# Optimization experiments

Measured on AMD Instinct MI355X. Metric: run time of the kernel, lower is better.

Reference implementation:

```python
import jax, jax.numpy as jnp
import numpy as np

B, S, D = 2, 2048, 4096
NH, NKV = 32, 8
HD = D // NH  # 128
N_REP = NH // NKV  # 4


def setup_inputs() -> dict:
    key = jax.random.key(0)
    ks = jax.random.split(key, 5)
    scale = 0.02
    return {
        "x": jax.random.normal(ks[0], (B, S, D), dtype=jnp.float32),
        "wq": jax.random.normal(ks[1], (D, NH * HD), dtype=jnp.float32) * scale,
        "wk": jax.random.normal(ks[2], (D, NKV * HD), dtype=jnp.float32) * scale,
        "wv": jax.random.normal(ks[3], (D, NKV * HD), dtype=jnp.float32) * scale,
        "wo": jax.random.normal(ks[4], (NH * HD, D), dtype=jnp.float32) * scale,
    }


def reference(x, wq, wk, wv, wo):
    bsz, toks, _ = x.shape
    q = (x @ wq).reshape(bsz, toks, NH, HD)      # [B,S,NH,HD]
    k = (x @ wk).reshape(bsz, toks, NKV, HD)     # [B,S,NKV,HD]
    v = (x @ wv).reshape(bsz, toks, NKV, HD)
    # GQA: fold n_rep into einsum instead of materializing repeated K/V.
    qg = q.reshape(bsz, toks, NKV, N_REP, HD)    # group query heads per kv head
    scores = jnp.einsum('bqgrd,bkgd->bgrqk', qg, k) / jnp.sqrt(jnp.asarray(HD, x.dtype))
    attn = jax.nn.softmax(scores.astype(jnp.float32), axis=-1).astype(x.dtype)
    out = jnp.einsum('bgrqk,bkgd->bqgrd', attn, v)  # [B,S,NKV,N_REP,HD]
    out = out.reshape(bsz, toks, NH * HD)
    return out @ wo
```

## Files before the change

### kernel.cpp

```cpp
#include <hip/hip_runtime.h>
#include <math.h>

typedef _Float16 f16;
using f16x8 = __attribute__((ext_vector_type(8))) _Float16;
using f32x4 = __attribute__((ext_vector_type(4))) float;

#define BATCH 2
#define SEQ   2048
#define DMODEL 4096
#define NH    32
#define NKV   8
#define HD    128
#define MTOK  (BATCH*SEQ)

__global__ __launch_bounds__(256) void prep_k(const float* __restrict__ x, f16* __restrict__ xh,
                                              const float* __restrict__ wq, f16* __restrict__ wqT,
                                              const float* __restrict__ wk, const float* __restrict__ wv,
                                              f16* __restrict__ wkvT,
                                              const float* __restrict__ wo, f16* __restrict__ woT,
                                              float scale) {
  __shared__ float tile[32][33];
  const int bid = blockIdx.x, t = threadIdx.x;
  if (bid < 8192) {
    const int i = bid * 256 + t;
    const float4* p = reinterpret_cast<const float4*>(x) + (size_t)i * 2;
    float4 a = p[0], b = p[1];
    f16x8 o = { (f16)a.x, (f16)a.y, (f16)a.z, (f16)a.w,
                (f16)b.x, (f16)b.y, (f16)b.z, (f16)b.w };
    reinterpret_cast<f16x8*>(xh)[i] = o;
    return;
  }
  const float* w; f16* dst; int Nd; float sc;
  int bb;
  if (bid < 24576)      { bb = bid - 8192;  w = wq; dst = wqT;  Nd = DMODEL; sc = scale; }
  else if (bid < 32768) { bb = bid - 24576; const int z = bb >> 12; bb &= 4095;
                          w = z ? wv : wk; dst = wkvT + (size_t)z * 1024 * DMODEL; Nd = 1024; sc = 1.0f; }
  else                  { bb = bid - 32768; w = wo; dst = woT; Nd = DMODEL; sc = 1.0f; }
  const int ntile = Nd >> 5;
  const int n0 = (bb % ntile) * 32, k0 = (bb / ntile) * 32;
  const int r = t >> 3, c4 = (t & 7) << 2;
  const float4 v = *reinterpret_cast<const float4*>(w + (size_t)(k0 + r) * Nd + n0 + c4);
  tile[r][c4 + 0] = v.x; tile[r][c4 + 1] = v.y; tile[r][c4 + 2] = v.z; tile[r][c4 + 3] = v.w;
  __syncthreads();
  union { f16 h[4]; ushort4 u4; } pk;
  pk.h[0] = (f16)(tile[c4 + 0][r] * sc);
  pk.h[1] = (f16)(tile[c4 + 1][r] * sc);
  pk.h[2] = (f16)(tile[c4 + 2][r] * sc);
  pk.h[3] = (f16)(tile[c4 + 3][r] * sc);
  *reinterpret_cast<ushort4*>(dst + (size_t)(n0 + r) * DMODEL + k0 + c4) = pk.u4;
}

__global__ __launch_bounds__(256) void transpose_cvt_k(const float* __restrict__ w,
                                                       f16* __restrict__ wt, int Kd, int Nd,
                                                       float scale) {
  __shared__ float tile[32][33];
  const int t = threadIdx.x;
  const int n0 = blockIdx.x * 32, k0 = blockIdx.y * 32;
  const int r = t >> 3, c4 = (t & 7) << 2;
  const float4 v = *reinterpret_cast<const float4*>(w + (size_t)(k0 + r) * Nd + n0 + c4);
  tile[r][c4 + 0] = v.x; tile[r][c4 + 1] = v.y; tile[r][c4 + 2] = v.z; tile[r][c4 + 3] = v.w;
  __syncthreads();
  union { f16 h[4]; ushort4 u4; } pk;
  pk.h[0] = (f16)(tile[c4 + 0][r] * scale);
  pk.h[1] = (f16)(tile[c4 + 1][r] * scale);
  pk.h[2] = (f16)(tile[c4 + 2][r] * scale);
  pk.h[3] = (f16)(tile[c4 + 3][r] * scale);
  *reinterpret_cast<ushort4*>(wt + (size_t)(n0 + r) * Kd + k0 + c4) = pk.u4;
}

__global__ __launch_bounds__(256) void transpose_cvt2_k(const float* __restrict__ w0,
                                                        const float* __restrict__ w1,
                                                        f16* __restrict__ wt, int Kd, int Nd) {
  __shared__ float tile[32][33];
  const float* w = blockIdx.z ? w1 : w0;
  f16* dst = wt + (size_t)blockIdx.z * Nd * Kd;
  const int t = threadIdx.x;
  const int n0 = blockIdx.x * 32, k0 = blockIdx.y * 32;
  const int r = t >> 3, c4 = (t & 7) << 2;
  const float4 v = *reinterpret_cast<const float4*>(w + (size_t)(k0 + r) * Nd + n0 + c4);
  tile[r][c4 + 0] = v.x; tile[r][c4 + 1] = v.y; tile[r][c4 + 2] = v.z; tile[r][c4 + 3] = v.w;
  __syncthreads();
  union { f16 h[4]; ushort4 u4; } pk;
  pk.h[0] = (f16)tile[c4 + 0][r];
  pk.h[1] = (f16)tile[c4 + 1][r];
  pk.h[2] = (f16)tile[c4 + 2][r];
  pk.h[3] = (f16)tile[c4 + 3][r];
  *reinterpret_cast<ushort4*>(dst + (size_t)(n0 + r) * Kd + k0 + c4) = pk.u4;
}

__global__ __launch_bounds__(256) void cvt_f32_f16_k(const float* __restrict__ in,
                                                     f16* __restrict__ out, int n8) {
  int i = blockIdx.x * 256 + threadIdx.x;
  if (i >= n8) return;
  const float4* p = reinterpret_cast<const float4*>(in) + (size_t)i * 2;
  float4 a = p[0], b = p[1];
  f16x8 o = { (f16)a.x, (f16)a.y, (f16)a.z, (f16)a.w,
              (f16)b.x, (f16)b.y, (f16)b.z, (f16)b.w };
  reinterpret_cast<f16x8*>(out)[i] = o;
}

__global__ __launch_bounds__(512, 2) void gemm_kv8_k(const f16* __restrict__ A,
                                                     const f16* __restrict__ BT,
                                                     f16* __restrict__ Kc,
                                                     f16* __restrict__ Vt,
                                                     int M, int N, int K) {
  __shared__ f16 lds[2 * 24576];
  char* ldsb = (char*)lds;

  const int t = threadIdx.x, lane = t & 63, w = t >> 6;
  const int wm = w >> 2, wn = w & 3;
  const int ll = lane & 15, lg = lane >> 4;
  const int nbn = N >> 8;
  const int nwg = gridDim.x, cpx = nwg >> 3, bid = blockIdx.x;
  const int swz = (bid & 7) * cpx + (bid >> 3);
  const int bm = swz / nbn, bn = swz % nbn;
  const size_t m0 = (size_t)bm << 7, n0 = (size_t)bn << 8;
  const int NT = K >> 6;

  const int uoff[4] = {0, 8192, 16384, 32768};

  auto stage = [&](int bufI, int unit, int ktS) {
    char* dstb = ldsb + (size_t)bufI * 49152 + uoff[unit];
    if (unit < 2) {
      const f16* base = A + (m0 + (size_t)(unit & 1) * 64) * (size_t)K;
      const int row = t >> 3, lin = t & 7;
      const int slot = lin ^ (row & 7);
      const f16* src = base + (size_t)row * K + ktS + slot * 8;
      __builtin_amdgcn_global_load_lds((const __attribute__((address_space(1))) void*)src,
          (__attribute__((address_space(3))) void*)(dstb + (size_t)t * 16), 16, 0, 0);
    } else {
      const f16* base = BT + (n0 + (size_t)(unit & 1) * 128) * (size_t)K;
#pragma unroll
      for (int rr = 0; rr < 2; rr++) {
        const int u = t + rr * 512;
        const int row = u >> 3, lin = u & 7;
        const int slot = lin ^ (row & 7);
        const f16* src = base + (size_t)row * K + ktS + slot * 8;
        __builtin_amdgcn_global_load_lds((const __attribute__((address_space(1))) void*)src,
            (__attribute__((address_space(3))) void*)(dstb + (size_t)u * 16), 16, 0, 0);
      }
    }
  };

  f32x4 acc[4][4];
#pragma unroll
  for (int i = 0; i < 4; i++)
#pragma unroll
    for (int j = 0; j < 4; j++) acc[i][j] = f32x4{0.f, 0.f, 0.f, 0.f};

  f16x8 af[2][2];
  f16x8 bfr[2][2][2];

  stage(0, 0, 0); stage(0, 1, 0); stage(0, 2, 0); stage(0, 3, 0);
  stage(1, 0, 64); stage(1, 2, 64); stage(1, 3, 64);
  asm volatile("s_waitcnt vmcnt(5)" ::: "memory");
  __builtin_amdgcn_sched_barrier(0);
  __builtin_amdgcn_s_barrier();

#define PHK(RBUF, RDA, RDB, SBUF, SUNIT, STILE, VM, MH, NHQ) do {                         \
    if ((RDA) >= 0) {                                                                     \
      const char* ab = ldsb + (size_t)(RBUF) * 49152 + uoff[MH];                          \
      _Pragma("unroll") for (int mi2 = 0; mi2 < 2; mi2++)                                 \
        _Pragma("unroll") for (int kk = 0; kk < 2; kk++) {                                \
          const int ri = wm * 32 + mi2 * 16 + ll;                                         \
          af[mi2][kk] = *reinterpret_cast<const f16x8*>(ab + ri * 128                     \
                               + ((((kk << 2) + lg) ^ (ri & 7)) << 4));                   \
        }                                                                                 \
    }                                                                                     \
    if ((RDB) >= 0) {                                                                     \
      const char* bb = ldsb + (size_t)(RBUF) * 49152 + uoff[2 + (RDB)];                   \
      _Pragma("unroll") for (int ni2 = 0; ni2 < 2; ni2++)                                 \
        _Pragma("unroll") for (int kk = 0; kk < 2; kk++) {                                \
          const int ri = wn * 32 + ni2 * 16 + ll;                                         \
          bfr[RDB][ni2][kk] = *reinterpret_cast<const f16x8*>(bb + ri * 128               \
                               + ((((kk << 2) + lg) ^ (ri & 7)) << 4));                   \
        }                                                                                 \
    }                                                                                     \
    stage((SBUF), (SUNIT), ((STILE) & (NT - 1)) << 6);                                    \
    if (VM) { asm volatile("s_waitcnt vmcnt(5)" ::: "memory");                            \
              __builtin_amdgcn_sched_barrier(0); }                                        \
    __builtin_amdgcn_s_barrier();                                                         \
    asm volatile("s_waitcnt lgkmcnt(0)" ::: "memory");                                    \
    __builtin_amdgcn_sched_barrier(0);                                                    \
    __builtin_amdgcn_s_setprio(1);                                                        \
    _Pragma("unroll") for (int kk = 0; kk < 2; kk++)                                      \
      _Pragma("unroll") for (int mi2 = 0; mi2 < 2; mi2++)                                 \
        _Pragma("unroll") for (int ni2 = 0; ni2 < 2; ni2++)                               \
          acc[(MH) * 2 + mi2][(NHQ) * 2 + ni2] = __builtin_amdgcn_mfma_f32_16x16x32_f16(  \
              af[mi2][kk], bfr[NHQ][ni2][kk], acc[(MH) * 2 + mi2][(NHQ) * 2 + ni2],       \
              0, 0, 0);                                                                   \
    __builtin_amdgcn_s_setprio(0);                                                        \
    __builtin_amdgcn_s_barrier();                                                         \
  } while (0)

  for (int tt = 0; tt < NT; tt += 2) {
    PHK(0,  0,  0, 1, 1, tt + 1, false, 0, 0);
    PHK(0, -1,  1, 0, 0, tt + 2, false, 0, 1);
    PHK(0,  1, -1, 0, 2, tt + 2, false, 1, 0);
    PHK(0, -1, -1, 0, 3, tt + 2, true , 1, 1);
    PHK(1,  0,  0, 0, 1, tt + 2, false, 0, 0);
    PHK(1, -1,  1, 1, 0, tt + 3, false, 0, 1);
    PHK(1,  1, -1, 1, 2, tt + 3, false, 1, 0);
    PHK(1, -1, -1, 1, 3, tt + 3, true , 1, 1);
  }
#undef PHK

#pragma unroll
  for (int mh = 0; mh < 2; mh++)
#pragma unroll
    for (int mi2 = 0; mi2 < 2; mi2++) {
      const size_t r0 = m0 + mh * 64 + wm * 32 + mi2 * 16 + lg * 4;
#pragma unroll
      for (int nh = 0; nh < 2; nh++)
#pragma unroll
        for (int ni2 = 0; ni2 < 2; ni2++) {
          const size_t c = n0 + nh * 128 + wn * 32 + ni2 * 16 + ll;
          const f32x4 v = acc[mh * 2 + mi2][nh * 2 + ni2];
          if ((int)c < 1024) {
#pragma unroll
            for (int rr = 0; rr < 4; rr++) Kc[(r0 + rr) * 1024 + c] = (f16)v[rr];
          } else {
            const int nc = (int)c - 1024;
            const int kvh = nc >> 7, d = nc & 127;
            const int b = (int)(r0 >> 11), sc = (int)(r0 & 2047);
            union { f16 h[4]; ushort4 u4; } pk;
#pragma unroll
            for (int rr = 0; rr < 4; rr++) pk.h[rr] = (f16)v[rr];
            *reinterpret_cast<ushort4*>(Vt + (((size_t)(b * NKV + kvh) * HD + d) * SEQ + sc)) = pk.u4;
          }
        }
    }
}

template<int MODE>
__global__ __launch_bounds__(512, 2) void gemm256_k(const f16* __restrict__ A,
                                                    const f16* __restrict__ BT,
                                                    void* __restrict__ Cv,
                                                    int M, int N, int K) {
  __shared__ f16 lds[2 * 4 * 128 * 64];
  char* ldsb = (char*)lds;

  const int t = threadIdx.x, lane = t & 63, w = t >> 6;
  const int wm = w >> 2, wn = w & 3;
  const int ll = lane & 15, lg = lane >> 4;
  const int nbn = N >> 8;
  const int nwg = gridDim.x, cpx = nwg >> 3, bid = blockIdx.x;
  const int swz = (bid & 7) * cpx + (bid >> 3);
  const int bm = swz / nbn, bn = swz % nbn;
  const size_t m0 = (size_t)bm << 8, n0 = (size_t)bn << 8;
  const int NT = K >> 6;

  auto stage = [&](int bufI, int unit, int ktS) {
    const f16* base = (unit < 2) ? (A + (m0 + (size_t)(unit & 1) * 128) * (size_t)K)
                                 : (BT + (n0 + (size_t)(unit & 1) * 128) * (size_t)K);
#pragma unroll
    for (int rr = 0; rr < 2; rr++) {
      const int u = t + rr * 512;
      const int row = u >> 3, lin = u & 7;
      const int slot = lin ^ (row & 7);
      const f16* src = base + (size_t)row * K + ktS + slot * 8;
      char* dst = ldsb + (size_t)(bufI * 4 + unit) * 16384 + (size_t)(w * 64 + rr * 512) * 16;
      __builtin_amdgcn_global_load_lds((const __attribute__((address_space(1))) void*)src,
          (__attribute__((address_space(3))) void*)dst, 16, 0, 0);
    }
  };

  f32x4 acc[8][4];
#pragma unroll
  for (int i = 0; i < 8; i++)
#pragma unroll
    for (int j = 0; j < 4; j++) acc[i][j] = f32x4{0.f, 0.f, 0.f, 0.f};

  f16x8 af[4][2];
  f16x8 bfr[2][2][2];

  stage(0, 0, 0); stage(0, 2, 0); stage(0, 3, 0); stage(0, 1, 0);
  stage(1, 0, 64); stage(1, 2, 64); stage(1, 3, 64);
  asm volatile("s_waitcnt vmcnt(6)" ::: "memory");
  __builtin_amdgcn_sched_barrier(0);
  __builtin_amdgcn_s_barrier();

#define PH(RBUF, RDA, RDB, SBUF, SUNIT, STILE, VM, MH, NHQ) do {                          \
    if ((RDA) >= 0) {                                                                     \
      const char* ab = ldsb + (size_t)((RBUF) * 4 + (RDA)) * 16384;                       \
      _Pragma("unroll") for (int mi = 0; mi < 4; mi++)                                    \
        _Pragma("unroll") for (int kk = 0; kk < 2; kk++)                                  \
          af[mi][kk] = *reinterpret_cast<const f16x8*>(ab + (mi * 32 + wm * 16 + ll) * 128\
                               + ((((kk << 2) + lg) ^ (ll & 7)) << 4));                   \
    }                                                                                     \
    if ((RDB) >= 0) {                                                                     \
      const char* bb = ldsb + (size_t)((RBUF) * 4 + 2 + (RDB)) * 16384;                   \
      _Pragma("unroll") for (int ni = 0; ni < 2; ni++)                                    \
        _Pragma("unroll") for (int kk = 0; kk < 2; kk++)                                  \
          bfr[RDB][ni][kk] = *reinterpret_cast<const f16x8*>(bb +                         \
                               (wn * 32 + ni * 16 + ll) * 128                             \
                               + ((((kk << 2) + lg) ^ (ll & 7)) << 4));                   \
    }                                                                                     \
    stage((SBUF), (SUNIT), ((STILE) & (NT - 1)) << 6);                                    \
    if ((RDA) >= 0 && (RDB) >= 0)                                                         \
      asm volatile("s_waitcnt lgkmcnt(8)" ::: "memory");     \
    if (VM) { asm volatile("s_waitcnt vmcnt(6)" ::: "memory");                            \
              __builtin_amdgcn_sched_barrier(0); }                                        \
    __builtin_amdgcn_s_barrier();                                                         \
    asm volatile("s_waitcnt lgkmcnt(0)" ::: "memory");                                    \
    __builtin_amdgcn_sched_barrier(0);                                                    \
    __builtin_amdgcn_s_setprio(1);                                                        \
    _Pragma("unroll") for (int kk = 0; kk < 2; kk++)                                      \
      _Pragma("unroll") for (int mi = 0; mi < 4; mi++)                                    \
        _Pragma("unroll") for (int ni = 0; ni < 2; ni++)                                  \
          acc[(MH) * 4 + mi][(NHQ) * 2 + ni] = __builtin_amdgcn_mfma_f32_16x16x32_f16(    \
              af[mi][kk], bfr[NHQ][ni][kk], acc[(MH) * 4 + mi][(NHQ) * 2 + ni], 0, 0, 0); \
    __builtin_amdgcn_s_setprio(0);                                                        \
    __builtin_amdgcn_s_barrier();                                                         \
  } while (0)

  for (int tt = 0; tt < NT; tt += 2) {
    PH(0,  0,  0, 1, 1, tt + 1, false, 0, 0);
    PH(0, -1,  1, 0, 0, tt + 2, false, 0, 1);
    PH(0,  1, -1, 0, 2, tt + 2, false, 1, 0);
    PH(0, -1, -1, 0, 3, tt + 2, true , 1, 1);
    PH(1,  0,  0, 0, 1, tt + 2, false, 0, 0);
    PH(1, -1,  1, 1, 0, tt + 3, false, 0, 1);
    PH(1,  1, -1, 1, 2, tt + 3, false, 1, 0);
    PH(1, -1, -1, 1, 3, tt + 3, true , 1, 1);
  }
#undef PH

#pragma unroll
  for (int mh = 0; mh < 2; mh++)
#pragma unroll
    for (int mi = 0; mi < 4; mi++) {
      const size_t r0 = m0 + mh * 128 + mi * 32 + wm * 16 + lg * 4;
#pragma unroll
      for (int nh = 0; nh < 2; nh++)
#pragma unroll
        for (int ni = 0; ni < 2; ni++) {
          const size_t c = n0 + nh * 128 + wn * 32 + ni * 16 + ll;
          const f32x4 v = acc[mh * 4 + mi][nh * 2 + ni];
          if (MODE == 0) {
            f16* C = (f16*)Cv;
#pragma unroll
            for (int rr = 0; rr < 4; rr++) C[(r0 + rr) * N + c] = (f16)v[rr];
          } else {
            float* C = (float*)Cv;
#pragma unroll
            for (int rr = 0; rr < 4; rr++) C[(r0 + rr) * N + c] = v[rr];
          }
        }
    }
}

__global__ __launch_bounds__(512) void attn_k11(const f16* __restrict__ Q,
                                                const f16* __restrict__ Kb,
                                                const f16* __restrict__ VT,
                                                f16* __restrict__ ctx) {
  __shared__ f16 Klds[2][64 * 128];
  __shared__ f16 Vlds[2][128 * 64];
  __shared__ f16 Plds[8][16 * 64];

  const int t = threadIdx.x, lane = t & 63, w = t >> 6;
  const int bid = blockIdx.x;
  const int swz = (bid & 7) * 128 + (bid >> 3);
  const int qt = swz & 63, kvh = (swz >> 6) & 7, b = swz >> 9;
  const int h = kvh * 4 + (w & 3);
  const int q0 = qt * 32 + (w >> 2) * 16;
  const int ll = lane & 15, lg = lane >> 4;

  const f16* Qb = Q + ((size_t)(b * SEQ + q0) * NH + h) * HD;
  const f16* Kh = Kb + ((size_t)b * SEQ * NKV + kvh) * HD;
  const f16* Vh = VT + ((size_t)(b * NKV + kvh)) * HD * SEQ;

  f16x8 qf[4];
#pragma unroll
  for (int kd = 0; kd < 4; kd++)
    qf[kd] = *reinterpret_cast<const f16x8*>(Qb + (size_t)ll * (NH * HD) + kd * 32 + lg * 8);

  float m_ = -INFINITY;
  float l_ = 0.f;
  f32x4 o[8];
#pragma unroll
  for (int df = 0; df < 8; df++) o[df] = f32x4{0.f, 0.f, 0.f, 0.f};

  const float THR = 11.5416f;

  auto stage = [&](int bufi, int kt) {
#pragma unroll
    for (int rr = 0; rr < 2; rr++) {
      const int u = w * 128 + rr * 64 + lane;
      const int krow = u >> 4, klin = u & 15;
      const int kslot = klin ^ (krow & 7);
      const f16* ksrc = Kh + (size_t)(kt + krow) * (NKV * HD) + kslot * 8;
      __builtin_amdgcn_global_load_lds((const __attribute__((address_space(1))) void*)ksrc,
          (__attribute__((address_space(3))) void*)((char*)&Klds[bufi][0] + (size_t)u * 16), 16, 0, 0);
      const int vrow = u >> 3, vlin = u & 7;
      const int vslot = vlin ^ (vrow & 7);
      const f16* vsrc = Vh + (size_t)vrow * SEQ + kt + vslot * 8;
      __builtin_amdgcn_global_load_lds((const __attribute__((address_space(1))) void*)vsrc,
          (__attribute__((address_space(3))) void*)((char*)&Vlds[bufi][0] + (size_t)u * 16), 16, 0, 0);
    }
  };

  stage(0, 0);
  __syncthreads();

  for (int kt = 0; kt < SEQ; kt += 64) {
    const int buf = (kt >> 6) & 1;
    if (kt + 64 < SEQ) stage(buf ^ 1, kt + 64);

    const char* Kt = (const char*)Klds[buf];
    const char* Vt = (const char*)Vlds[buf];

    f32x4 s[4];
    __builtin_amdgcn_s_setprio(1);
#pragma unroll
    for (int nf = 0; nf < 4; nf++) {
      f32x4 a = f32x4{0.f, 0.f, 0.f, 0.f};
#pragma unroll
      for (int kd = 0; kd < 4; kd++) {
        const int row = nf * 16 + ll;
        f16x8 kf = *reinterpret_cast<const f16x8*>(
            Kt + row * 256 + ((((kd << 2) + lg) ^ (row & 7)) << 4));
        a = __builtin_amdgcn_mfma_f32_16x16x32_f16(kf, qf[kd], a, 0, 0, 0);
      }
      s[nf] = a;
    }
    __builtin_amdgcn_s_setprio(0);

    float mx = s[0][0];
#pragma unroll
    for (int nf = 0; nf < 4; nf++)
#pragma unroll
      for (int r = 0; r < 4; r++) mx = fmaxf(mx, s[nf][r]);

    if (!__all((int)(mx <= m_ + THR))) {
      float mr = fmaxf(mx, __shfl_xor(mx, 16, 64));
      mr = fmaxf(mr, __shfl_xor(mr, 32, 64));
      const float mn = fmaxf(m_, mr);
      const float corrq = __builtin_amdgcn_exp2f(m_ - mn);
      m_ = mn;
      l_ *= corrq;
#pragma unroll
      for (int r = 0; r < 4; r++) {
        const float c = __shfl(corrq, (lane & 48) | (lg * 4 + r), 64);
#pragma unroll
        for (int df = 0; df < 8; df++) o[df][r] *= c;
      }
    }

    float rs = 0.f;
#pragma unroll
    for (int nf = 0; nf < 4; nf++)
#pragma unroll
      for (int r = 0; r < 4; r++) {
        const float p = __builtin_amdgcn_exp2f(s[nf][r] - m_);
        s[nf][r] = p;
        rs += p;
      }
    rs += __shfl_xor(rs, 16, 64);
    rs += __shfl_xor(rs, 32, 64);
    l_ += rs;

    char* Pw = (char*)&Plds[w][0];
#pragma unroll
    for (int nf = 0; nf < 4; nf++) {
      union { f16 h[4]; ushort4 u4; } pk;
#pragma unroll
      for (int r = 0; r < 4; r++) pk.h[r] = (f16)s[nf][r];
      *reinterpret_cast<ushort4*>(Pw + ll * 128 + ((nf * 32 + lg * 8) ^ ((ll & 7) << 4))) = pk.u4;
    }

    f16x8 pf[2];
#pragma unroll
    for (int kf = 0; kf < 2; kf++)
      pf[kf] = *reinterpret_cast<const f16x8*>(Pw + ll * 128 + (((kf << 6) + (lg << 4)) ^ ((ll & 7) << 4)));

    __builtin_amdgcn_s_setprio(1);
#pragma unroll
    for (int kf = 0; kf < 2; kf++)
#pragma unroll
      for (int df = 0; df < 8; df++) {
        const int row = df * 16 + ll;
        f16x8 vf = *reinterpret_cast<const f16x8*>(
            Vt + row * 128 + ((((kf << 2) + lg) ^ (row & 7)) << 4));
        o[df] = __builtin_amdgcn_mfma_f32_16x16x32_f16(pf[kf], vf, o[df], 0, 0, 0);
      }
    __builtin_amdgcn_s_setprio(0);

    __syncthreads();
  }

  float inv[4];
#pragma unroll
  for (int r = 0; r < 4; r++) {
    const float lq = __shfl(l_, (lane & 48) | (lg * 4 + r), 64);
    inv[r] = 1.0f / lq;
  }
  f16* cb = ctx + ((size_t)(b * SEQ + q0) * NH + h) * HD;
#pragma unroll
  for (int df = 0; df < 8; df++)
#pragma unroll
    for (int r = 0; r < 4; r++)
      cb[(size_t)(lg * 4 + r) * (NH * HD) + df * 16 + ll] = (f16)(o[df][r] * inv[r]);
}

extern "C" void kernel_launch(void* const* d_in, const int* in_sizes, int n_in,
                              void* d_out, int out_size, void* d_ws, size_t ws_size,
                              hipStream_t stream) {
  (void)in_sizes; (void)n_in; (void)out_size;
  const float* x  = (const float*)d_in[0];
  const float* wq = (const float*)d_in[1];
  const float* wk = (const float*)d_in[2];
  const float* wv = (const float*)d_in[3];
  const float* wo = (const float*)d_in[4];
  float* out = (float*)d_out;

  const size_t SZ_X   = (size_t)MTOK * DMODEL * sizeof(f16);
  const size_t SZ_KV  = (size_t)MTOK * NKV * HD * sizeof(f16);
  const size_t SZ_WKV = (size_t)2048 * DMODEL * sizeof(f16);
  const size_t BASE   = 3 * SZ_X + 2 * SZ_KV;
  if (ws_size < BASE) return;

  char* ws = (char*)d_ws;
  f16* xh   = (f16*)ws;
  f16* wT   = (f16*)(ws + SZ_X);
  f16* Qb   = (f16*)(ws + 2 * SZ_X);
  f16* Kb   = (f16*)(ws + 3 * SZ_X);
  f16* VTb  = (f16*)(ws + 3 * SZ_X + SZ_KV);
  f16* wkvT = (f16*)(ws + BASE);
  f16* woT  = (f16*)(ws + BASE + SZ_WKV);

  const float KSC2 = 0.08838834764831845f * 1.4426950408889634f;

  const bool pathA = ws_size >= BASE + SZ_WKV + SZ_X;
  const bool pathB = !pathA && ws_size >= BASE + SZ_WKV;

  if (pathA || pathB) {
    const int grid = pathA ? 49152 : 32768;
    prep_k<<<dim3(grid), 256, 0, stream>>>(x, xh, wq, wT, wk, wv, wkvT, wo, woT, KSC2);
    gemm256_k<0><<<dim3((MTOK / 256) * (DMODEL / 256)), 512, 0, stream>>>(xh, wT, Qb, MTOK, DMODEL, DMODEL);
    gemm_kv8_k<<<dim3((MTOK / 128) * (2048 / 256)), 512, 0, stream>>>(xh, wkvT, Kb, VTb, MTOK, 2048, DMODEL);
    attn_k11<<<dim3(BATCH * NKV * (SEQ / 32)), 512, 0, stream>>>(Qb, Kb, VTb, xh);
    if (pathA) {
      gemm256_k<2><<<dim3((MTOK / 256) * (DMODEL / 256)), 512, 0, stream>>>(xh, woT, out, MTOK, DMODEL, DMODEL);
    } else {
      transpose_cvt_k<<<dim3(DMODEL / 32, DMODEL / 32), 256, 0, stream>>>(wo, wT, DMODEL, DMODEL, 1.0f);
      gemm256_k<2><<<dim3((MTOK / 256) * (DMODEL / 256)), 512, 0, stream>>>(xh, wT, out, MTOK, DMODEL, DMODEL);
    }
  } else {
    cvt_f32_f16_k<<<dim3(MTOK * DMODEL / 8 / 256), 256, 0, stream>>>(x, xh, MTOK * DMODEL / 8);
    transpose_cvt_k<<<dim3(DMODEL / 32, DMODEL / 32), 256, 0, stream>>>(wq, wT, DMODEL, DMODEL, KSC2);
    gemm256_k<0><<<dim3((MTOK / 256) * (DMODEL / 256)), 512, 0, stream>>>(xh, wT, Qb, MTOK, DMODEL, DMODEL);
    transpose_cvt2_k<<<dim3(NKV * HD / 32, DMODEL / 32, 2), 256, 0, stream>>>(wk, wv, wT, DMODEL, NKV * HD);
    gemm_kv8_k<<<dim3((MTOK / 128) * (2048 / 256)), 512, 0, stream>>>(xh, wT, Kb, VTb, MTOK, 2048, DMODEL);
    attn_k11<<<dim3(BATCH * NKV * (SEQ / 32)), 512, 0, stream>>>(Qb, Kb, VTb, xh);
    transpose_cvt_k<<<dim3(DMODEL / 32, DMODEL / 32), 256, 0, stream>>>(wo, wT, DMODEL, DMODEL, 1.0f);
    gemm256_k<2><<<dim3((MTOK / 256) * (DMODEL / 256)), 512, 0, stream>>>(xh, wT, out, MTOK, DMODEL, DMODEL);
  }
}
```

Measured before the change: 522.2 us.

## Fuse Q and KV projection GEMMs into one launch with block-range dispatch

Adds a combined QKV projection kernel whose first 256 blocks compute the Q projection with 256x256 tiles and whose remaining 256 blocks compute K and transposed V with 128x256 tiles. On the large-workspace path this replaces two back-to-back GEMM launches with one. The aim is to remove the tail and launch gap between the Q and KV GEMMs so both fill the GPU concurrently. The LDS buffer is sized for the larger branch, which may limit occupancy for the KV blocks, and the two block types have unequal work.

```diff
diff --git a/kernel.cpp b/kernel.cpp
--- a/kernel.cpp
+++ b/kernel.cpp
@@ -99,6 +99,245 @@
   reinterpret_cast<f16x8*>(out)[i] = o;
 }
 
+__global__ __launch_bounds__(512, 2) void gemm_qkv_k(const f16* __restrict__ A,
+                                                     const f16* __restrict__ wqT, f16* __restrict__ Qb,
+                                                     const f16* __restrict__ wkvT,
+                                                     f16* __restrict__ Kc, f16* __restrict__ Vt) {
+  __shared__ __align__(16) char ldsb_raw[131072];
+  char* ldsb = ldsb_raw;
+
+  const int bid0 = blockIdx.x;
+  const int t = threadIdx.x, lane = t & 63, w = t >> 6;
+  const int wm = w >> 2, wn = w & 3;
+  const int ll = lane & 15, lg = lane >> 4;
+  const int M = MTOK, K = DMODEL;
+  const int NT = K >> 6;
+
+  if (bid0 < 256) {
+    const f16* BT = wqT;
+    const int N = DMODEL;
+    const int nbn = N >> 8;
+    const int cpx = 256 >> 3, bid = bid0;
+    const int swz = (bid & 7) * cpx + (bid >> 3);
+    const int bm = swz / nbn, bn = swz % nbn;
+    const size_t m0 = (size_t)bm << 8, n0 = (size_t)bn << 8;
+
+    auto stage = [&](int bufI, int unit, int ktS) {
+      const f16* base = (unit < 2) ? (A + (m0 + (size_t)(unit & 1) * 128) * (size_t)K)
+                                   : (BT + (n0 + (size_t)(unit & 1) * 128) * (size_t)K);
+#pragma unroll
+      for (int rr = 0; rr < 2; rr++) {
+        const int u = t + rr * 512;
+        const int row = u >> 3, lin = u & 7;
+        const int slot = lin ^ (row & 7);
+        const f16* src = base + (size_t)row * K + ktS + slot * 8;
+        char* dst = ldsb + (size_t)(bufI * 4 + unit) * 16384 + (size_t)(w * 64 + rr * 512) * 16;
+        __builtin_amdgcn_global_load_lds((const __attribute__((address_space(1))) void*)src,
+            (__attribute__((address_space(3))) void*)dst, 16, 0, 0);
+      }
+    };
+
+    f32x4 acc[8][4];
+#pragma unroll
+    for (int i = 0; i < 8; i++)
+#pragma unroll
+      for (int j = 0; j < 4; j++) acc[i][j] = f32x4{0.f, 0.f, 0.f, 0.f};
+
+    f16x8 af[4][2];
+    f16x8 bfr[2][2][2];
+
+    stage(0, 0, 0); stage(0, 2, 0); stage(0, 3, 0); stage(0, 1, 0);
+    stage(1, 0, 64); stage(1, 2, 64); stage(1, 3, 64);
+    asm volatile("s_waitcnt vmcnt(6)" ::: "memory");
+    __builtin_amdgcn_sched_barrier(0);
+    __builtin_amdgcn_s_barrier();
+
+#define PH(RBUF, RDA, RDB, SBUF, SUNIT, STILE, VM, MH, NHQ) do {                          \
+    if ((RDA) >= 0) {                                                                     \
+      const char* ab = ldsb + (size_t)((RBUF) * 4 + (RDA)) * 16384;                       \
+      _Pragma("unroll") for (int mi = 0; mi < 4; mi++)                                    \
+        _Pragma("unroll") for (int kk = 0; kk < 2; kk++)                                  \
+          af[mi][kk] = *reinterpret_cast<const f16x8*>(ab + (mi * 32 + wm * 16 + ll) * 128\
+                               + ((((kk << 2) + lg) ^ (ll & 7)) << 4));                   \
+    }                                                                                     \
+    if ((RDB) >= 0) {                                                                     \
+      const char* bb = ldsb + (size_t)((RBUF) * 4 + 2 + (RDB)) * 16384;                   \
+      _Pragma("unroll") for (int ni = 0; ni < 2; ni++)                                    \
+        _Pragma("unroll") for (int kk = 0; kk < 2; kk++)                                  \
+          bfr[RDB][ni][kk] = *reinterpret_cast<const f16x8*>(bb +                         \
+                               (wn * 32 + ni * 16 + ll) * 128                             \
+                               + ((((kk << 2) + lg) ^ (ll & 7)) << 4));                   \
+    }                                                                                     \
+    stage((SBUF), (SUNIT), ((STILE) & (NT - 1)) << 6);                                    \
+    if ((RDA) >= 0 && (RDB) >= 0)                                                         \
+      asm volatile("s_waitcnt lgkmcnt(8)" ::: "memory");                                  \
+    if (VM) { asm volatile("s_waitcnt vmcnt(6)" ::: "memory");                            \
+              __builtin_amdgcn_sched_barrier(0); }                                        \
+    __builtin_amdgcn_s_barrier();                                                         \
+    asm volatile("s_waitcnt lgkmcnt(0)" ::: "memory");                                    \
+    __builtin_amdgcn_sched_barrier(0);                                                    \
+    __builtin_amdgcn_s_setprio(1);                                                        \
+    _Pragma("unroll") for (int kk = 0; kk < 2; kk++)                                      \
+      _Pragma("unroll") for (int mi = 0; mi < 4; mi++)                                    \
+        _Pragma("unroll") for (int ni = 0; ni < 2; ni++)                                  \
+          acc[(MH) * 4 + mi][(NHQ) * 2 + ni] = __builtin_amdgcn_mfma_f32_16x16x32_f16(    \
+              af[mi][kk], bfr[NHQ][ni][kk], acc[(MH) * 4 + mi][(NHQ) * 2 + ni], 0, 0, 0); \
+    __builtin_amdgcn_s_setprio(0);                                                        \
+    __builtin_amdgcn_s_barrier();                                                         \
+  } while (0)
+
+    for (int tt = 0; tt < NT; tt += 2) {
+      PH(0,  0,  0, 1, 1, tt + 1, false, 0, 0);
+      PH(0, -1,  1, 0, 0, tt + 2, false, 0, 1);
+      PH(0,  1, -1, 0, 2, tt + 2, false, 1, 0);
+      PH(0, -1, -1, 0, 3, tt + 2, true , 1, 1);
+      PH(1,  0,  0, 0, 1, tt + 2, false, 0, 0);
+      PH(1, -1,  1, 1, 0, tt + 3, false, 0, 1);
+      PH(1,  1, -1, 1, 2, tt + 3, false, 1, 0);
+      PH(1, -1, -1, 1, 3, tt + 3, true , 1, 1);
+    }
+#undef PH
+
+#pragma unroll
+    for (int mh = 0; mh < 2; mh++)
+#pragma unroll
+      for (int mi = 0; mi < 4; mi++) {
+        const size_t r0 = m0 + mh * 128 + mi * 32 + wm * 16 + lg * 4;
+#pragma unroll
+        for (int nh = 0; nh < 2; nh++)
+#pragma unroll
+          for (int ni = 0; ni < 2; ni++) {
+            const size_t c = n0 + nh * 128 + wn * 32 + ni * 16 + ll;
+            const f32x4 v = acc[mh * 4 + mi][nh * 2 + ni];
+#pragma unroll
+            for (int rr = 0; rr < 4; rr++) Qb[(r0 + rr) * N + c] = (f16)v[rr];
+          }
+      }
+  } else {
+    const f16* BT = wkvT;
+    const int N = 2048;
+    const int nbn = N >> 8;
+    const int cpx = 256 >> 3, bid = bid0 - 256;
+    const int swz = (bid & 7) * cpx + (bid >> 3);
+    const int bm = swz / nbn, bn = swz % nbn;
+    const size_t m0 = (size_t)bm << 7, n0 = (size_t)bn << 8;
+
+    const int uoff[4] = {0, 8192, 16384, 32768};
+
+    auto stage = [&](int bufI, int unit, int ktS) {
+      char* dstb = ldsb + (size_t)bufI * 49152 + uoff[unit];
+      if (unit < 2) {
+        const f16* base = A + (m0 + (size_t)(unit & 1) * 64) * (size_t)K;
+        const int row = t >> 3, lin = t & 7;
+        const int slot = lin ^ (row & 7);
+        const f16* src = base + (size_t)row * K + ktS + slot * 8;
+        __builtin_amdgcn_global_load_lds((const __attribute__((address_space(1))) void*)src,
+            (__attribute__((address_space(3))) void*)(dstb + (size_t)t * 16), 16, 0, 0);
+      } else {
+        const f16* base = BT + (n0 + (size_t)(unit & 1) * 128) * (size_t)K;
+#pragma unroll
+        for (int rr = 0; rr < 2; rr++) {
+          const int u = t + rr * 512;
+          const int row = u >> 3, lin = u & 7;
+          const int slot = lin ^ (row & 7);
+          const f16* src = base + (size_t)row * K + ktS + slot * 8;
+          __builtin_amdgcn_global_load_lds((const __attribute__((address_space(1))) void*)src,
+              (__attribute__((address_space(3))) void*)(dstb + (size_t)u * 16), 16, 0, 0);
+        }
+      }
+    };
+
+    f32x4 acc[4][4];
+#pragma unroll
+    for (int i = 0; i < 4; i++)
+#pragma unroll
+      for (int j = 0; j < 4; j++) acc[i][j] = f32x4{0.f, 0.f, 0.f, 0.f};
+
+    f16x8 af[2][2];
+    f16x8 bfr[2][2][2];
+
+    stage(0, 0, 0); stage(0, 1, 0); stage(0, 2, 0); stage(0, 3, 0);
+    stage(1, 0, 64); stage(1, 2, 64); stage(1, 3, 64);
+    asm volatile("s_waitcnt vmcnt(5)" ::: "memory");
+    __builtin_amdgcn_sched_barrier(0);
+    __builtin_amdgcn_s_barrier();
+
+#define PHK(RBUF, RDA, RDB, SBUF, SUNIT, STILE, VM, MH, NHQ) do {                         \
+    if ((RDA) >= 0) {                                                                     \
+      const char* ab = ldsb + (size_t)(RBUF) * 49152 + uoff[MH];                          \
+      _Pragma("unroll") for (int mi2 = 0; mi2 < 2; mi2++)                                 \
+        _Pragma("unroll") for (int kk = 0; kk < 2; kk++) {                                \
+          const int ri = wm * 32 + mi2 * 16 + ll;                                         \
+          af[mi2][kk] = *reinterpret_cast<const f16x8*>(ab + ri * 128                     \
+                               + ((((kk << 2) + lg) ^ (ri & 7)) << 4));                   \
+        }                                                                                 \
+    }                                                                                     \
+    if ((RDB) >= 0) {                                                                     \
+      const char* bb = ldsb + (size_t)(RBUF) * 49152 + uoff[2 + (RDB)];                   \
+      _Pragma("unroll") for (int ni2 = 0; ni2 < 2; ni2++)                                 \
+        _Pragma("unroll") for (int kk = 0; kk < 2; kk++) {                                \
+          const int ri = wn * 32 + ni2 * 16 + ll;                                         \
+          bfr[RDB][ni2][kk] = *reinterpret_cast<const f16x8*>(bb + ri * 128               \
+                               + ((((kk << 2) + lg) ^ (ri & 7)) << 4));                   \
+        }                                                                                 \
+    }                                                                                     \
+    stage((SBUF), (SUNIT), ((STILE) & (NT - 1)) << 6);                                    \
+    if (VM) { asm volatile("s_waitcnt vmcnt(5)" ::: "memory");                            \
+              __builtin_amdgcn_sched_barrier(0); }                                        \
+    __builtin_amdgcn_s_barrier();                                                        \
+    asm volatile("s_waitcnt lgkmcnt(0)" ::: "memory");                                    \
+    __builtin_amdgcn_sched_barrier(0);                                                    \
+    __builtin_amdgcn_s_setprio(1);                                                        \
+    _Pragma("unroll") for (int kk = 0; kk < 2; kk++)                                      \
+      _Pragma("unroll") for (int mi2 = 0; mi2 < 2; mi2++)                                 \
+        _Pragma("unroll") for (int ni2 = 0; ni2 < 2; ni2++)                               \
+          acc[(MH) * 2 + mi2][(NHQ) * 2 + ni2] = __builtin_amdgcn_mfma_f32_16x16x32_f16(  \
+              af[mi2][kk], bfr[NHQ][ni2][kk], acc[(MH) * 2 + mi2][(NHQ) * 2 + ni2],       \
+              0, 0, 0);                                                                   \
+    __builtin_amdgcn_s_setprio(0);                                                        \
+    __builtin_amdgcn_s_barrier();                                                        \
+  } while (0)
+
+    for (int tt = 0; tt < NT; tt += 2) {
+      PHK(0,  0,  0, 1, 1, tt + 1, false, 0, 0);
+      PHK(0, -1,  1, 0, 0, tt + 2, false, 0, 1);
+      PHK(0,  1, -1, 0, 2, tt + 2, false, 1, 0);
+      PHK(0, -1, -1, 0, 3, tt + 2, true , 1, 1);
+      PHK(1,  0,  0, 0, 1, tt + 2, false, 0, 0);
+      PHK(1, -1,  1, 1, 0, tt + 3, false, 0, 1);
+      PHK(1,  1, -1, 1, 2, tt + 3, false, 1, 0);
+      PHK(1, -1, -1, 1, 3, tt + 3, true , 1, 1);
+    }
+#undef PHK
+
+#pragma unroll
+    for (int mh = 0; mh < 2; mh++)
+#pragma unroll
+      for (int mi2 = 0; mi2 < 2; mi2++) {
+        const size_t r0 = m0 + mh * 64 + wm * 32 + mi2 * 16 + lg * 4;
+#pragma unroll
+        for (int nh = 0; nh < 2; nh++)
+#pragma unroll
+          for (int ni2 = 0; ni2 < 2; ni2++) {
+            const size_t c = n0 + nh * 128 + wn * 32 + ni2 * 16 + ll;
+            const f32x4 v = acc[mh * 2 + mi2][nh * 2 + ni2];
+            if ((int)c < 1024) {
+#pragma unroll
+              for (int rr = 0; rr < 4; rr++) Kc[(r0 + rr) * 1024 + c] = (f16)v[rr];
+            } else {
+              const int nc = (int)c - 1024;
+              const int kvh = nc >> 7, d = nc & 127;
+              const int b = (int)(r0 >> 11), sc = (int)(r0 & 2047);
+              union { f16 h[4]; ushort4 u4; } pk;
+#pragma unroll
+              for (int rr = 0; rr < 4; rr++) pk.h[rr] = (f16)v[rr];
+              *reinterpret_cast<ushort4*>(Vt + (((size_t)(b * NKV + kvh) * HD + d) * SEQ + sc)) = pk.u4;
+            }
+          }
+      }
+  }
+}
+
 __global__ __launch_bounds__(512, 2) void gemm_kv8_k(const f16* __restrict__ A,
                                                      const f16* __restrict__ BT,
                                                      f16* __restrict__ Kc,
@@ -190,7 +429,7 @@
               af[mi2][kk], bfr[NHQ][ni2][kk], acc[(MH) * 2 + mi2][(NHQ) * 2 + ni2],       \
               0, 0, 0);                                                                   \
     __builtin_amdgcn_s_setprio(0);                                                        \
-    __builtin_amdgcn_s_barrier();                                                         \
+    __builtin_amdgcn_s_barrier();                                                        \
   } while (0)
 
   for (int tt = 0; tt < NT; tt += 2) {
@@ -298,7 +537,7 @@
     }                                                                                     \
     stage((SBUF), (SUNIT), ((STILE) & (NT - 1)) << 6);                                    \
     if ((RDA) >= 0 && (RDB) >= 0)                                                         \
-      asm volatile("s_waitcnt lgkmcnt(8)" ::: "memory");     \
+      asm volatile("s_waitcnt lgkmcnt(8)" ::: "memory");                                  \
     if (VM) { asm volatile("s_waitcnt vmcnt(6)" ::: "memory");                            \
               __builtin_amdgcn_sched_barrier(0); }                                        \
     __builtin_amdgcn_s_barrier();                                                         \
@@ -311,7 +550,7 @@
           acc[(MH) * 4 + mi][(NHQ) * 2 + ni] = __builtin_amdgcn_mfma_f32_16x16x32_f16(    \
               af[mi][kk], bfr[NHQ][ni][kk], acc[(MH) * 4 + mi][(NHQ) * 2 + ni], 0, 0, 0); \
     __builtin_amdgcn_s_setprio(0);                                                        \
-    __builtin_amdgcn_s_barrier();                                                         \
+    __builtin_amdgcn_s_barrier();                                                        \
   } while (0)
 
   for (int tt = 0; tt < NT; tt += 2) {
@@ -350,7 +589,7 @@
     }
 }
 
-__global__ __launch_bounds__(512) void attn_k11(const f16* __restrict__ Q,
+__global__ __launch_bounds__(512) void attn_k12(const f16* __restrict__ Q,
                                                 const f16* __restrict__ Kb,
                                                 const f16* __restrict__ VT,
                                                 f16* __restrict__ ctx) {
@@ -534,25 +773,25 @@
   const bool pathA = ws_size >= BASE + SZ_WKV + SZ_X;
   const bool pathB = !pathA && ws_size >= BASE + SZ_WKV;
 
-  if (pathA || pathB) {
-    const int grid = pathA ? 49152 : 32768;
-    prep_k<<<dim3(grid), 256, 0, stream>>>(x, xh, wq, wT, wk, wv, wkvT, wo, woT, KSC2);
+  if (pathA) {
+    prep_k<<<dim3(49152), 256, 0, stream>>>(x, xh, wq, wT, wk, wv, wkvT, wo, woT, KSC2);
+    gemm_qkv_k<<<dim3(512), 512, 0, stream>>>(xh, wT, Qb, wkvT, Kb, VTb);
+    attn_k12<<<dim3(BATCH * NKV * (SEQ / 32)), 512, 0, stream>>>(Qb, Kb, VTb, xh);
+    gemm256_k<2><<<dim3((MTOK / 256) * (DMODEL / 256)), 512, 0, stream>>>(xh, woT, out, MTOK, DMODEL, DMODEL);
+  } else if (pathB) {
+    prep_k<<<dim3(32768), 256, 0, stream>>>(x, xh, wq, wT, wk, wv, wkvT, wo, woT, KSC2);
     gemm256_k<0><<<dim3((MTOK / 256) * (DMODEL / 256)), 512, 0, stream>>>(xh, wT, Qb, MTOK, DMODEL, DMODEL);
     gemm_kv8_k<<<dim3((MTOK / 128) * (2048 / 256)), 512, 0, stream>>>(xh, wkvT, Kb, VTb, MTOK, 2048, DMODEL);
-    attn_k11<<<dim3(BATCH * NKV * (SEQ / 32)), 512, 0, stream>>>(Qb, Kb, VTb, xh);
-    if (pathA) {
-      gemm256_k<2><<<dim3((MTOK / 256) * (DMODEL / 256)), 512, 0, stream>>>(xh, woT, out, MTOK, DMODEL, DMODEL);
-    } else {
-      transpose_cvt_k<<<dim3(DMODEL / 32, DMODEL / 32), 256, 0, stream>>>(wo, wT, DMODEL, DMODEL, 1.0f);
-      gemm256_k<2><<<dim3((MTOK / 256) * (DMODEL / 256)), 512, 0, stream>>>(xh, wT, out, MTOK, DMODEL, DMODEL);
-    }
+    attn_k12<<<dim3(BATCH * NKV * (SEQ / 32)), 512, 0, stream>>>(Qb, Kb, VTb, xh);
+    transpose_cvt_k<<<dim3(DMODEL / 32, DMODEL / 32), 256, 0, stream>>>(wo, wT, DMODEL, DMODEL, 1.0f);
+    gemm256_k<2><<<dim3((MTOK / 256) * (DMODEL / 256)), 512, 0, stream>>>(xh, wT, out, MTOK, DMODEL, DMODEL);
   } else {
     cvt_f32_f16_k<<<dim3(MTOK * DMODEL / 8 / 256), 256, 0, stream>>>(x, xh, MTOK * DMODEL / 8);
     transpose_cvt_k<<<dim3(DMODEL / 32, DMODEL / 32), 256, 0, stream>>>(wq, wT, DMODEL, DMODEL, KSC2);
     gemm256_k<0><<<dim3((MTOK / 256) * (DMODEL / 256)), 512, 0, stream>>>(xh, wT, Qb, MTOK, DMODEL, DMODEL);
     transpose_cvt2_k<<<dim3(NKV * HD / 32, DMODEL / 32, 2), 256, 0, stream>>>(wk, wv, wT, DMODEL, NKV * HD);
     gemm_kv8_k<<<dim3((MTOK / 128) * (2048 / 256)), 512, 0, stream>>>(xh, wT, Kb, VTb, MTOK, 2048, DMODEL);
-    attn_k11<<<dim3(BATCH * NKV * (SEQ / 32)), 512, 0, stream>>>(Qb, Kb, VTb, xh);
+    attn_k12<<<dim3(BATCH * NKV * (SEQ / 32)), 512, 0, stream>>>(Qb, Kb, VTb, xh);
     transpose_cvt_k<<<dim3(DMODEL / 32, DMODEL / 32), 256, 0, stream>>>(wo, wT, DMODEL, DMODEL, 1.0f);
     gemm256_k<2><<<dim3((MTOK / 256) * (DMODEL / 256)), 512, 0, stream>>>(xh, wT, out, MTOK, DMODEL, DMODEL);
   }
```

After: 518.3 us. About the same (-0.7%).
